# Kernel optimization log

Hardware: AMD Instinct MI355X
Metric: run time of the kernel (lower is better)

## Reference

```python
import jax, jax.numpy as jnp
import numpy as np

B, S, D, H, DFF, NB = 32, 512, 256, 8, 1024, 2
L = NB + 2 * NB  # 2 blocks_1 + 4 blocks_2 = 6 layers, params stacked on axis 0
DK = D // H
NEG = jnp.float32(-1e32)


def _ln(x, s, b):
    mu = jnp.mean(x, -1, keepdims=True)
    var = jnp.mean((x - mu) ** 2, -1, keepdims=True)
    return (x - mu) * jax.lax.rsqrt(var + 1e-5) * s + b


def _attn(q, k, v, gamma, mask, zero_pad):
    # q,k,v: [B,H,S,DK]; mask: [1,1,S,S] bool; gamma: [H,1,1]
    scores = jnp.einsum('bhid,bhjd->bhij', q, k) / jnp.float32(np.sqrt(DK))
    # distance-decay effect (computed with no grad in the original)
    sc = jax.nn.softmax(jnp.where(mask, scores, NEG), axis=-1) * mask
    cum = jnp.cumsum(sc, axis=-1)
    tot = jnp.sum(sc, axis=-1, keepdims=True)
    idx = jnp.arange(S, dtype=jnp.float32)
    pos = jnp.abs(idx[None, :] - idx[:, None])[None, None]  # |i-j|
    dist = jax.lax.stop_gradient(jnp.sqrt(jnp.maximum((tot - cum) * pos, 0.0)))
    g = -jax.nn.softplus(gamma)[None]  # [1,H,1,1]
    eff = jnp.clip(jnp.exp(dist * g), 1e-5, 1e5)
    scores = jnp.where(mask, scores * eff, NEG)
    a = jax.nn.softmax(scores, axis=-1)
    if zero_pad:
        a = a.at[:, :, 0, :].set(0.0)
    return jnp.einsum('bhij,bhjd->bhid', a, v)


def _layer(i, mask_flag, q, k, v, apply_pos,
           Wk, bk, Wv, bv, Wo, bo, gammas, ln1_s, ln1_b, W1, b1, W2, b2, ln2_s, ln2_b):
    diag = 0 if mask_flag == 1 else -1  # mask=1: incl. diag; mask=0: strictly past
    mask = jnp.tril(jnp.ones((S, S), bool), diag)[None, None]
    to_h = lambda x, W, bb: (x @ W + bb).reshape(B, S, H, DK).transpose(0, 2, 1, 3)
    qh = to_h(q, Wk[i], bk[i])  # kq_same=True -> q uses k_linear
    kh = to_h(k, Wk[i], bk[i])
    vh = to_h(v, Wv[i], bv[i])
    o = _attn(qh, kh, vh, gammas[i], mask, zero_pad=(mask_flag == 0))
    o = o.transpose(0, 2, 1, 3).reshape(B, S, D) @ Wo[i] + bo[i]
    q = _ln(q + o, ln1_s[i], ln1_b[i])
    if apply_pos:
        f = jax.nn.relu(q @ W1[i] + b1[i]) @ W2[i] + b2[i]
        q = _ln(q + f, ln2_s[i], ln2_b[i])
    return q


def _forward(q_embed_data, qa_embed_data, *p):
    y, x = qa_embed_data, q_embed_data
    for i in range(NB):
        y = _layer(i, 1, y, y, y, True, *p)
    flag = True
    for j in range(2 * NB):
        i = NB + j
        if flag:
            x = _layer(i, 1, x, x, x, False, *p)
        else:
            x = _layer(i, 0, x, x, y, True, *p)
        flag = not flag
    return x


def setup_inputs() -> dict:
    key = jax.random.key(0)
    ks = jax.random.split(key, 9)
    sd = jnp.float32(1.0 / np.sqrt(D))
    sdf = jnp.float32(1.0 / np.sqrt(DFF))
    xb = float(np.sqrt(3.0))  # xavier bound for gammas (fan_in=fan_out=1)
    return {
        'q_embed_data': jax.random.normal(ks[0], (B, S, D), jnp.float32),
        'qa_embed_data': jax.random.normal(ks[1], (B, S, D), jnp.float32),
        'Wk': jax.random.normal(ks[2], (L, D, D), jnp.float32) * sd,
        'bk': jnp.zeros((L, D), jnp.float32),
        'Wv': jax.random.normal(ks[3], (L, D, D), jnp.float32) * sd,
        'bv': jnp.zeros((L, D), jnp.float32),
        'Wo': jax.random.normal(ks[4], (L, D, D), jnp.float32) * sd,
        'bo': jnp.zeros((L, D), jnp.float32),
        'gammas': jax.random.uniform(ks[5], (L, H, 1, 1), jnp.float32, -xb, xb),
        'ln1_s': jnp.ones((L, D), jnp.float32),
        'ln1_b': jnp.zeros((L, D), jnp.float32),
        'W1': jax.random.normal(ks[6], (L, D, DFF), jnp.float32) * sd,
        'b1': jnp.zeros((L, DFF), jnp.float32),
        'W2': jax.random.normal(ks[7], (L, DFF, D), jnp.float32) * sdf,
        'b2': jnp.zeros((L, D), jnp.float32),
        'ln2_s': jnp.ones((L, D), jnp.float32),
        'ln2_b': jnp.zeros((L, D), jnp.float32),
    }


def reference(q_embed_data, qa_embed_data, Wk, bk, Wv, bv, Wo, bo, gammas,
              ln1_s, ln1_b, W1, b1, W2, b2, ln2_s, ln2_b):
    return _forward(q_embed_data, qa_embed_data, Wk, bk, Wv, bv, Wo, bo, gammas,
                    ln1_s, ln1_b, W1, b1, W2, b2, ln2_s, ln2_b)
```

## Files before the change

kernel.cpp:

```cpp
#include <hip/hip_runtime.h>
#include <cstdint>
#include <cstddef>


#define AS1 __attribute__((address_space(1)))
#define AS3 __attribute__((address_space(3)))

typedef __bf16 bf16;
typedef __bf16 bf16x8 __attribute__((ext_vector_type(8)));
typedef __bf16 bf16x4 __attribute__((ext_vector_type(4)));
typedef __bf16 bf16x2 __attribute__((ext_vector_type(2)));
typedef float  f32x4  __attribute__((ext_vector_type(4)));
typedef float  f32x16 __attribute__((ext_vector_type(16)));
typedef unsigned int u32;

static constexpr int Mc = 32 * 512;

__global__ void cvt_copy2_kernel(const float* __restrict__ s0, float* __restrict__ da32,
                                 bf16* __restrict__ da16, const float* __restrict__ s1,
                                 float* __restrict__ db32, bf16* __restrict__ db16, int n4) {
  const float* s = blockIdx.y ? s1 : s0;
  float* d32 = blockIdx.y ? db32 : da32;
  bf16* d16 = blockIdx.y ? db16 : da16;
  int i = blockIdx.x * blockDim.x + threadIdx.x;
  if (i < n4) {
    float4 v = ((const float4*)s)[i];
    ((float4*)d32)[i] = v;
    bf16x4 hx = {(bf16)v.x, (bf16)v.y, (bf16)v.z, (bf16)v.w};
    ((bf16x4*)d16)[i] = hx;
  }
}

__global__ __launch_bounds__(256) void transpose_cvt_all(
    const float* __restrict__ Wk, const float* __restrict__ Wv, const float* __restrict__ Wo,
    const float* __restrict__ W1, const float* __restrict__ W2,
    bf16* __restrict__ Wkt, bf16* __restrict__ Wvt, bf16* __restrict__ Wot,
    bf16* __restrict__ W1t, bf16* __restrict__ W2t) {
  int z = blockIdx.z;
  int layer = z % 6, w = z / 6;
  const float* src; bf16* dst; int K, N;
  switch (w) {
    case 0: src = Wk; dst = Wkt; K = 256; N = 256; break;
    case 1: src = Wv; dst = Wvt; K = 256; N = 256; break;
    case 2: src = Wo; dst = Wot; K = 256; N = 256; break;
    case 3: src = W1; dst = W1t; K = 256; N = 1024; break;
    default: src = W2; dst = W2t; K = 1024; N = 256; break;
  }
  int k0 = blockIdx.x * 64, n0 = blockIdx.y * 64;
  if (k0 >= K || n0 >= N) return;
  src += (size_t)layer * K * N;
  dst += (size_t)layer * K * N;
  __shared__ bf16 t[64][68];
  int tid = threadIdx.x;
  int rr = tid >> 4;
  int c4 = (tid & 15) * 4;
#pragma unroll
  for (int p = 0; p < 4; ++p) {
    int k = rr + p * 16;
    float4 v = *(const float4*)(src + (size_t)(k0 + k) * N + n0 + c4);
    t[c4 + 0][k] = (bf16)v.x;
    t[c4 + 1][k] = (bf16)v.y;
    t[c4 + 2][k] = (bf16)v.z;
    t[c4 + 3][k] = (bf16)v.w;
  }
  __syncthreads();
#pragma unroll
  for (int p = 0; p < 4; ++p) {
    int nl = rr + p * 16;
    bf16x4 o4 = *(const bf16x4*)&t[nl][c4];
    *(bf16x4*)(dst + (size_t)(n0 + nl) * K + k0 + c4) = o4;
  }
}

template <int RELU, typename OUT_T>
__device__ __forceinline__ void gemm_body(
    const bf16* __restrict__ A, const bf16* __restrict__ Bt,
    const float* __restrict__ bias, OUT_T* __restrict__ C,
    int K, int N, int m0, int n0, bf16* As, bf16* Bs) {
  const int tid = threadIdx.x;
  const int lane = tid & 63;
  const int wid = tid >> 6;
  const int wm = (wid >> 1) * 64;
  const int wn = (wid & 1) * 64;
  f32x4 acc[4][4] = {};

  const int o1 = wid * 1024 + lane * 16;
  const int o2 = o1 + 4096;
  const int r1 = o1 >> 6, c1 = o1 & 63;
  const int r2 = o2 >> 6, c2 = o2 & 63;
  const char* Ab = (const char*)A;
  const char* Bb = (const char*)Bt;
  const size_t stride = (size_t)K * 2;

  auto stage = [&](int buf, int kk) {
    const char* a1 = Ab + (size_t)(m0 + r1) * stride + (size_t)kk * 2 + c1;
    const char* a2 = Ab + (size_t)(m0 + r2) * stride + (size_t)kk * 2 + c2;
    const char* b1 = Bb + (size_t)(n0 + r1) * stride + (size_t)kk * 2 + c1;
    const char* b2 = Bb + (size_t)(n0 + r2) * stride + (size_t)kk * 2 + c2;
    char* ad = (char*)As + buf * 8192 + wid * 1024;
    char* bd = (char*)Bs + buf * 8192 + wid * 1024;
    __builtin_amdgcn_global_load_lds((const AS1 u32*)a1, (AS3 u32*)ad, 16, 0, 0);
    __builtin_amdgcn_global_load_lds((const AS1 u32*)a2, (AS3 u32*)(ad + 4096), 16, 0, 0);
    __builtin_amdgcn_global_load_lds((const AS1 u32*)b1, (AS3 u32*)bd, 16, 0, 0);
    __builtin_amdgcn_global_load_lds((const AS1 u32*)b2, (AS3 u32*)(bd + 4096), 16, 0, 0);
  };

  stage(0, 0);
  asm volatile("s_waitcnt vmcnt(0)" ::: "memory");
  __syncthreads();

  int cur = 0;
  for (int k0 = 0; k0 < K; k0 += 32) {
    if (k0 + 32 < K) stage(cur ^ 1, k0 + 32);
    const int rr = lane & 15;
    const int g8 = (lane >> 4) * 8;
    const int base = cur * 4096;
    bf16x8 af[4], bfr[4];
#pragma unroll
    for (int i = 0; i < 4; ++i) {
      af[i]  = *(const bf16x8*)&As[base + (wm + i * 16 + rr) * 32 + g8];
      bfr[i] = *(const bf16x8*)&Bs[base + (wn + i * 16 + rr) * 32 + g8];
    }
#pragma unroll
    for (int mi = 0; mi < 4; ++mi)
#pragma unroll
      for (int ni = 0; ni < 4; ++ni)
        acc[mi][ni] = __builtin_amdgcn_mfma_f32_16x16x32_bf16(af[mi], bfr[ni], acc[mi][ni], 0, 0, 0);
    asm volatile("s_waitcnt vmcnt(0)" ::: "memory");
    __syncthreads();
    cur ^= 1;
  }

  const int rr = lane & 15;
  const int g4 = (lane >> 4) * 4;
  float bv[4];
#pragma unroll
  for (int ni = 0; ni < 4; ++ni) bv[ni] = bias[n0 + wn + ni * 16 + rr];
#pragma unroll
  for (int mi = 0; mi < 4; ++mi)
#pragma unroll
    for (int ni = 0; ni < 4; ++ni)
#pragma unroll
      for (int r = 0; r < 4; ++r) {
        float v = acc[mi][ni][r] + bv[ni];
        if (RELU) v = fmaxf(v, 0.f);
        int row = m0 + wm + mi * 16 + g4 + r;
        int col = n0 + wn + ni * 16 + rr;
        C[(size_t)row * N + col] = (OUT_T)v;
      }
}

template <int RELU, typename OUT_T>
__global__ __launch_bounds__(256) void gemm_bias_kernel(
    const bf16* __restrict__ A, const bf16* __restrict__ Bt,
    const float* __restrict__ bias, OUT_T* __restrict__ C, int K, int N) {
  __shared__ bf16 As[2 * 128 * 32];
  __shared__ bf16 Bs[2 * 128 * 32];
  gemm_body<RELU, OUT_T>(A, Bt, bias, C, K, N, blockIdx.x * 128, blockIdx.y * 128, As, Bs);
}

__global__ __launch_bounds__(256) void gemm_kv_kernel(
    const bf16* __restrict__ A0, const bf16* __restrict__ Bt0,
    const float* __restrict__ b0, bf16* __restrict__ C0,
    const bf16* __restrict__ A1, const bf16* __restrict__ Bt1,
    const float* __restrict__ b1, bf16* __restrict__ C1, int K, int N) {
  __shared__ bf16 As[2 * 128 * 32];
  __shared__ bf16 Bs[2 * 128 * 32];
  int sel = blockIdx.y >> 1;
  gemm_body<0, bf16>(sel ? A1 : A0, sel ? Bt1 : Bt0, sel ? b1 : b0, sel ? C1 : C0,
                     K, N, blockIdx.x * 128, (blockIdx.y & 1) * 128, As, Bs);
}

template <int KSZ>
__global__ __launch_bounds__(512, 4) void gemm_ln_kernel(
    const bf16* __restrict__ A, const bf16* __restrict__ Bt,
    const float* __restrict__ bias, const float* __restrict__ resid,
    const float* __restrict__ lns, const float* __restrict__ lnb,
    float* __restrict__ out32, bf16* __restrict__ out16) {
  __shared__ bf16 As[2 * 32 * 32];
  __shared__ bf16 Bs[2 * 256 * 32];
  __shared__ float wsum[8][16][2];
  __shared__ float stats[32][2];
  const int tid = threadIdx.x, lane = tid & 63, wid = tid >> 6;
  const int m0 = blockIdx.x * 32;
  const int wr = wid >> 2, wc = wid & 3;
  f32x4 acc[4] = {};
  const char* Ab = (const char*)A;
  const char* Bb = (const char*)Bt;
  const size_t stride = (size_t)KSZ * 2;

  auto stage = [&](int buf, int kk) {
    if (wid < 2) {
      int off = wid * 1024 + lane * 16;
      const char* a1 = Ab + (size_t)(m0 + (off >> 6)) * stride + (size_t)kk * 2 + (off & 63);
      __builtin_amdgcn_global_load_lds((const AS1 u32*)a1,
                                       (AS3 u32*)((char*)As + buf * 2048 + wid * 1024), 16, 0, 0);
    }
    int off1 = wid * 2048 + lane * 16;
    int off2 = off1 + 1024;
    const char* b1 = Bb + (size_t)(off1 >> 6) * stride + (size_t)kk * 2 + (off1 & 63);
    const char* b2 = Bb + (size_t)(off2 >> 6) * stride + (size_t)kk * 2 + (off2 & 63);
    char* bd = (char*)Bs + buf * 16384 + wid * 2048;
    __builtin_amdgcn_global_load_lds((const AS1 u32*)b1, (AS3 u32*)bd, 16, 0, 0);
    __builtin_amdgcn_global_load_lds((const AS1 u32*)b2, (AS3 u32*)(bd + 1024), 16, 0, 0);
  };

  stage(0, 0);
  asm volatile("s_waitcnt vmcnt(0)" ::: "memory");
  __syncthreads();

  int cur = 0;
  for (int k0 = 0; k0 < KSZ; k0 += 32) {
    if (k0 + 32 < KSZ) stage(cur ^ 1, k0 + 32);
    const int rr = lane & 15, g8 = (lane >> 4) * 8;
    bf16x8 af = *(const bf16x8*)&As[cur * 1024 + (wr * 16 + rr) * 32 + g8];
    bf16x8 bfr[4];
#pragma unroll
    for (int ni = 0; ni < 4; ++ni)
      bfr[ni] = *(const bf16x8*)&Bs[cur * 8192 + (wc * 64 + ni * 16 + rr) * 32 + g8];
#pragma unroll
    for (int ni = 0; ni < 4; ++ni)
      acc[ni] = __builtin_amdgcn_mfma_f32_16x16x32_bf16(af, bfr[ni], acc[ni], 0, 0, 0);
    asm volatile("s_waitcnt vmcnt(0)" ::: "memory");
    __syncthreads();
    cur ^= 1;
  }

  const int rr = lane & 15, g4 = (lane >> 4) * 4;
  float bv[4], scv[4], biv[4];
  int col[4];
#pragma unroll
  for (int ni = 0; ni < 4; ++ni) {
    col[ni] = wc * 64 + ni * 16 + rr;
    bv[ni] = bias[col[ni]];
    scv[ni] = lns[col[ni]];
    biv[ni] = lnb[col[ni]];
  }
  float v[4][4];
#pragma unroll
  for (int r = 0; r < 4; ++r) {
    int grow = m0 + wr * 16 + g4 + r;
#pragma unroll
    for (int ni = 0; ni < 4; ++ni)
      v[ni][r] = acc[ni][r] + bv[ni] + resid[(size_t)grow * 256 + col[ni]];
  }
#pragma unroll
  for (int r = 0; r < 4; ++r) {
    float s1 = (v[0][r] + v[1][r]) + (v[2][r] + v[3][r]);
    float s2 = (v[0][r] * v[0][r] + v[1][r] * v[1][r]) + (v[2][r] * v[2][r] + v[3][r] * v[3][r]);
#pragma unroll
    for (int off = 8; off; off >>= 1) {
      s1 += __shfl_xor(s1, off);
      s2 += __shfl_xor(s2, off);
    }
    if (rr == 0) {
      int lrow = wr * 16 + g4 + r;
      wsum[wid][lrow & 15][0] = s1;
      wsum[wid][lrow & 15][1] = s2;
    }
  }
  __syncthreads();
  if (tid < 32) {
    int row = tid;
    int band = row >> 4;
    float s1 = 0.f, s2 = 0.f;
#pragma unroll
    for (int k = 0; k < 4; ++k) {
      s1 += wsum[band * 4 + k][row & 15][0];
      s2 += wsum[band * 4 + k][row & 15][1];
    }
    float mu = s1 * (1.f / 256.f);
    float var = s2 * (1.f / 256.f) - mu * mu;
    stats[row][0] = mu;
    stats[row][1] = rsqrtf(var + 1e-5f);
  }
  __syncthreads();
#pragma unroll
  for (int r = 0; r < 4; ++r) {
    int lrow = wr * 16 + g4 + r;
    int grow = m0 + lrow;
    float mu = stats[lrow][0], rs = stats[lrow][1];
#pragma unroll
    for (int ni = 0; ni < 4; ++ni) {
      float y = (v[ni][r] - mu) * rs * scv[ni] + biv[ni];
      out32[(size_t)grow * 256 + col[ni]] = y;
      out16[(size_t)grow * 256 + col[ni]] = (bf16)y;
    }
  }
}

static constexpr int LDK = 34;
static constexpr int LDV = 534;
static constexpr float LOG2E = 1.4426950408889634f;
static constexpr float KSC = 0.17677669529663687f * LOG2E;

__device__ __forceinline__ int jloc(int r, int hi) { return (r & 3) + 8 * (r >> 2) + 4 * hi; }

__device__ __forceinline__ u32 pkbf(float x, float y) {
  bf16x2 t = {(bf16)x, (bf16)y};
  return __builtin_bit_cast(u32, t);
}

__device__ __forceinline__ void plswap(u32& a, u32& b) {
  asm volatile("v_permlane32_swap_b32 %0, %1" : "+v"(a), "+v"(b));
}

__device__ __forceinline__ f32x16 qk_tile(const bf16* Klds, int jbase, int lq,
                                          const bf16x8& qf0, const bf16x8& qf1, int hi) {
  const bf16x8 ka0 = *(const bf16x8*)&Klds[(jbase + lq) * LDK + hi * 8];
  const bf16x8 ka1 = *(const bf16x8*)&Klds[(jbase + lq) * LDK + 16 + hi * 8];
  f32x16 c = {};
  c = __builtin_amdgcn_mfma_f32_32x32x16_bf16(ka0, qf0, c, 0, 0, 0);
  c = __builtin_amdgcn_mfma_f32_32x32x16_bf16(ka1, qf1, c, 0, 0, 0);
  return c;
}

template <bool MASKED>
__device__ __forceinline__ void tileA(const f32x16& c, int jbase, int hi, int qlim, float& tot) {
  float t[4] = {0.f, 0.f, 0.f, 0.f};
#pragma unroll
  for (int q2 = 0; q2 < 4; ++q2)
#pragma unroll
    for (int p = 0; p < 4; ++p) {
      const int r = q2 * 4 + p;
      float e = __builtin_amdgcn_exp2f(c[r] * KSC);
      if (MASKED) {
        int j = jbase + 8 * q2 + 4 * hi + p;
        if (j > qlim) e = 0.f;
      }
      t[q2] += e;
    }
  tot += (t[0] + t[1]) + (t[2] + t[3]);
}

template <bool MASKED>
__device__ __forceinline__ void tileB(const f32x16& c, int jbase, int lq, int hi,
                                      int qlim, float itot, float gneg2, float posf,
                                      const bf16* Vt, float& run, float& sum2, f32x16& pvacc) {
  float su2[16], lcs[16], G[4];
#pragma unroll
  for (int q2 = 0; q2 < 4; ++q2) {
    float a = 0.f;
#pragma unroll
    for (int p = 0; p < 4; ++p) {
      const int r = q2 * 4 + p;
      su2[r] = c[r] * KSC;
      float e = __builtin_amdgcn_exp2f(su2[r]);
      if (MASKED) {
        int j = jbase + 8 * q2 + 4 * hi + p;
        if (j > qlim) e = 0.f;
      }
      a += e;
      lcs[r] = a;
    }
    G[q2] = a;
  }
  float Po[4];
#pragma unroll
  for (int q2 = 0; q2 < 4; ++q2) Po[q2] = __shfl_xor(G[q2], 32);
  float base[4];
  {
    float pre = run;
#pragma unroll
    for (int q2 = 0; q2 < 4; ++q2) {
      base[q2] = pre + (hi ? Po[q2] : 0.f);
      pre += G[q2] + Po[q2];
    }
    run = pre;
  }
#pragma unroll
  for (int cc = 0; cc < 2; ++cc) {
    float pv[8];
#pragma unroll
    for (int q2s = 0; q2s < 2; ++q2s) {
      const int q2 = cc * 2 + q2s;
#pragma unroll
      for (int p = 0; p < 4; ++p) {
        const int r = q2 * 4 + p;
        float cum = base[q2] + lcs[r];
        float pos = posf - (float)(8 * q2 + p);
        float d2 = fmaxf(__builtin_fmaf(-cum, itot, 1.f) * pos, 0.f);
        float dist = __builtin_amdgcn_sqrtf(d2);
        float eff = fmaxf(__builtin_amdgcn_exp2f(dist * gneg2), 1e-5f);
        float t = __builtin_amdgcn_exp2f(su2[r] * eff);
        if (MASKED) {
          int j = jbase + 8 * q2 + 4 * hi + p;
          if (j > qlim) t = 0.f;
        }
        pv[q2s * 4 + p] = t;
      }
    }
    sum2 += ((pv[0] + pv[1]) + (pv[2] + pv[3])) + ((pv[4] + pv[5]) + (pv[6] + pv[7]));
    u32 a0 = pkbf(pv[0], pv[1]);
    u32 a1 = pkbf(pv[2], pv[3]);
    u32 b0 = pkbf(pv[4], pv[5]);
    u32 b1 = pkbf(pv[6], pv[7]);
    plswap(a0, b0);
    plswap(a1, b1);
    uint4 fq; fq.x = a0; fq.y = a1; fq.z = b0; fq.w = b1;
    bf16x8 pa = __builtin_bit_cast(bf16x8, fq);
    bf16x8 vb = *(const bf16x8*)&Vt[(size_t)lq * LDV + jbase + cc * 16 + hi * 8];
    pvacc = __builtin_amdgcn_mfma_f32_32x32x16_bf16(pa, vb, pvacc, 0, 0, 0);
  }
}

__global__ __launch_bounds__(1024, 4) void attn_kernel(
    const bf16* __restrict__ kh, const bf16* __restrict__ vh,
    const float* __restrict__ gam, bf16* __restrict__ o, int incl_diag) {
  __shared__ bf16 Klds[512 * LDK];
  __shared__ bf16 Vt[32 * LDV];

  const int tid = threadIdx.x;
  const int lane = tid & 63;
  const int wid = tid >> 6;
  const int bh = blockIdx.x;
  const int b = bh >> 3, h = bh & 7;
  const bf16* kbase = kh + ((size_t)b * 4096 + h) * 32;
  const bf16* vbase = vh + ((size_t)b * 4096 + h) * 32;
  bf16* obase = o + ((size_t)b * 4096 + h) * 32;

#pragma unroll
  for (int it = 0; it < 2; ++it) {
    int t = it * 1024 + tid;
    int j = t >> 2, cc = t & 3;
    bf16x8 kv8 = *(const bf16x8*)(kbase + (size_t)j * 256 + cc * 8);
    *(bf16x8*)&Klds[j * LDK + cc * 8] = kv8;
  }
  {
    int u = tid & 255;
    int cg = tid >> 8;
    const bf16* vb = vbase + (size_t)(2 * u) * 256 + cg * 8;
    bf16x8 r0 = *(const bf16x8*)(vb);
    bf16x8 r1 = *(const bf16x8*)(vb + 256);
#pragma unroll
    for (int e = 0; e < 8; ++e) {
      bf16x2 w2 = {r0[e], r1[e]};
      *(bf16x2*)&Vt[(size_t)(cg * 8 + e) * LDV + 2 * u] = w2;
    }
  }
  __syncthreads();

  float gm = gam[h];
  float gneg = -(fmaxf(gm, 0.f) + log1pf(__expf(-fabsf(gm))));
  const float gneg2 = gneg * LOG2E;
  const int lq = lane & 31;
  const int hi = lane >> 5;

  const int k = wid & 3, gsel = wid >> 2;
  int qb;
  switch (gsel) {
    case 0: qb = k; break;
    case 1: qb = 7 - k; break;
    case 2: qb = 8 + k; break;
    default: qb = 15 - k; break;
  }
  const int q0 = qb * 32;
  const int qr = q0 + lq;
  const int qlim = incl_diag ? qr : qr - 1;

  const bf16x8 qf0 = *(const bf16x8*)&Klds[(q0 + lq) * LDK + hi * 8];
  const bf16x8 qf1 = *(const bf16x8*)&Klds[(q0 + lq) * LDK + 16 + hi * 8];

  float tot = 0.f;
  {
    f32x16 c = qk_tile(Klds, 0, lq, qf0, qf1, hi);
    for (int jt = 0; jt < qb; ++jt) {
      f32x16 cn = qk_tile(Klds, (jt + 1) * 32, lq, qf0, qf1, hi);
      tileA<false>(c, jt * 32, hi, qlim, tot);
      c = cn;
    }
    tileA<true>(c, q0, hi, qlim, tot);
  }
  tot += __shfl_xor(tot, 32);
  const float itot = tot > 0.f ? 1.f / tot : 0.f;

  float run = 0.f, sum2 = 0.f;
  f32x16 pvacc = {};
  float posf = (float)(qr - 4 * hi);
  {
    f32x16 c = qk_tile(Klds, 0, lq, qf0, qf1, hi);
    for (int jt = 0; jt < qb; ++jt) {
      f32x16 cn = qk_tile(Klds, (jt + 1) * 32, lq, qf0, qf1, hi);
      tileB<false>(c, jt * 32, lq, hi, qlim, itot, gneg2, posf, Vt, run, sum2, pvacc);
      posf -= 32.f;
      c = cn;
    }
    tileB<true>(c, q0, lq, hi, qlim, itot, gneg2, posf, Vt, run, sum2, pvacc);
  }
  sum2 += __shfl_xor(sum2, 32);
  const float inv2 = sum2 > 0.f ? 1.f / sum2 : 0.f;

#pragma unroll
  for (int r = 0; r < 16; ++r) {
    int qv = jloc(r, hi);
    float iv = __shfl(inv2, qv);
    obase[(size_t)(q0 + qv) * 256 + lq] = (bf16)(pvacc[r] * iv);
  }
}

extern "C" void kernel_launch(void* const* d_in, const int* in_sizes, int n_in,
                              void* d_out, int out_size, void* d_ws, size_t ws_size,
                              hipStream_t stream) {
  const float* q_embed  = (const float*)d_in[0];
  const float* qa_embed = (const float*)d_in[1];
  const float* Wk = (const float*)d_in[2];
  const float* bk = (const float*)d_in[3];
  const float* Wv = (const float*)d_in[4];
  const float* bv = (const float*)d_in[5];
  const float* Wo = (const float*)d_in[6];
  const float* bo = (const float*)d_in[7];
  const float* gammas = (const float*)d_in[8];
  const float* ln1_s = (const float*)d_in[9];
  const float* ln1_b = (const float*)d_in[10];
  const float* W1 = (const float*)d_in[11];
  const float* b1 = (const float*)d_in[12];
  const float* W2 = (const float*)d_in[13];
  const float* b2 = (const float*)d_in[14];
  const float* ln2_s = (const float*)d_in[15];
  const float* ln2_b = (const float*)d_in[16];
  float* out = (float*)d_out;

  char* ws = (char*)d_ws;
  float* y32 = (float*)(ws);
  float* x32 = (float*)(ws + ((size_t)16 << 20));
  bf16* y16  = (bf16*)(ws + ((size_t)32 << 20));
  bf16* x16  = (bf16*)(ws + ((size_t)40 << 20));
  bf16* khb  = (bf16*)(ws + ((size_t)48 << 20));
  bf16* vhb  = (bf16*)(ws + ((size_t)56 << 20));
  bf16* o16  = (bf16*)(ws + ((size_t)64 << 20));
  bf16* h116 = (bf16*)(ws + ((size_t)88 << 20));
  bf16* Wkt  = (bf16*)(ws + ((size_t)122 << 20));
  bf16* Wvt  = Wkt + 6 * 65536;
  bf16* Wot  = Wvt + 6 * 65536;
  bf16* W1t  = Wot + 6 * 65536;
  bf16* W2t  = W1t + 6 * 262144;

  transpose_cvt_all<<<dim3(16, 16, 30), 256, 0, stream>>>(Wk, Wv, Wo, W1, W2,
                                                          Wkt, Wvt, Wot, W1t, W2t);
  cvt_copy2_kernel<<<dim3(4096, 2), 256, 0, stream>>>(q_embed, x32, x16,
                                                      qa_embed, y32, y16, Mc * 256 / 4);

  for (int i = 0; i < 6; ++i) {
    const bool first = (i < 2);
    const bool strict = (i == 3 || i == 5);
    const bool pos = first || strict;
    bf16* in16 = first ? y16 : x16;
    bf16* v16  = (first || strict) ? y16 : x16;
    float* res32 = first ? y32 : x32;

    gemm_kv_kernel<<<dim3(128, 4), 256, 0, stream>>>(
        in16, Wkt + (size_t)i * 65536, bk + i * 256, khb,
        v16, Wvt + (size_t)i * 65536, bv + i * 256, vhb, 256, 256);
    attn_kernel<<<256, 1024, 0, stream>>>(khb, vhb, gammas + i * 8, o16, strict ? 0 : 1);
    gemm_ln_kernel<256><<<512, 512, 0, stream>>>(
        o16, Wot + (size_t)i * 65536, bo + i * 256, res32,
        ln1_s + i * 256, ln1_b + i * 256, res32, in16);
    if (pos) {
      gemm_bias_kernel<1, bf16><<<dim3(128, 8), 256, 0, stream>>>(
          in16, W1t + (size_t)i * 262144, b1 + i * 1024, h116, 256, 1024);
      float* fin = (i == 5) ? out : res32;
      gemm_ln_kernel<1024><<<512, 512, 0, stream>>>(
          h116, W2t + (size_t)i * 262144, b2 + i * 256, res32,
          ln2_s + i * 256, ln2_b + i * 256, fin, in16);
    }
  }
}
```

Before: 614.7 us.

## Split high query tiles across wave pairs to balance causal attention work

Replaces the static wave-to-query-block assignment with a pairing scheme. Each front wave handles a low query block and also the first part of the key range for a high query block. The paired back wave handles the rest of that high block's key range. Partial row sums, normaliser sums and PV accumulators are exchanged through shared memory with two block barriers. This evens out per-wave work under the causal mask, at the cost of extra LDS (a 32x32 float tile per pair), extra barriers, and dropping the software prefetch of the next QK tile.

Measured after the change: 600.6 us. 2.3% less time.

```diff
diff --git a/kernel.cpp b/kernel.cpp
--- a/kernel.cpp
+++ b/kernel.cpp
@@ -409,6 +409,10 @@
     const float* __restrict__ gam, bf16* __restrict__ o, int incl_diag) {
   __shared__ bf16 Klds[512 * LDK];
   __shared__ bf16 Vt[32 * LDV];
+  __shared__ float exA[8][32];
+  __shared__ float exB[8][32];
+  __shared__ float s2A[8][32];
+  __shared__ float pvp[8][32][32];
 
   const int tid = threadIdx.x;
   const int lane = tid & 63;
@@ -446,55 +450,120 @@
   const int lq = lane & 31;
   const int hi = lane >> 5;
 
-  const int k = wid & 3, gsel = wid >> 2;
-  int qb;
-  switch (gsel) {
-    case 0: qb = k; break;
-    case 1: qb = 7 - k; break;
-    case 2: qb = 8 + k; break;
-    default: qb = 15 - k; break;
-  }
-  const int q0 = qb * 32;
-  const int qr = q0 + lq;
-  const int qlim = incl_diag ? qr : qr - 1;
-
-  const bf16x8 qf0 = *(const bf16x8*)&Klds[(q0 + lq) * LDK + hi * 8];
-  const bf16x8 qf1 = *(const bf16x8*)&Klds[(q0 + lq) * LDK + 16 + hi * 8];
-
-  float tot = 0.f;
-  {
-    f32x16 c = qk_tile(Klds, 0, lq, qf0, qf1, hi);
-    for (int jt = 0; jt < qb; ++jt) {
-      f32x16 cn = qk_tile(Klds, (jt + 1) * 32, lq, qf0, qf1, hi);
-      tileA<false>(c, jt * 32, hi, qlim, tot);
-      c = cn;
-    }
-    tileA<true>(c, q0, hi, qlim, tot);
-  }
-  tot += __shfl_xor(tot, 32);
-  const float itot = tot > 0.f ? 1.f / tot : 0.f;
-
-  float run = 0.f, sum2 = 0.f;
-  f32x16 pvacc = {};
-  float posf = (float)(qr - 4 * hi);
-  {
-    f32x16 c = qk_tile(Klds, 0, lq, qf0, qf1, hi);
-    for (int jt = 0; jt < qb; ++jt) {
-      f32x16 cn = qk_tile(Klds, (jt + 1) * 32, lq, qf0, qf1, hi);
-      tileB<false>(c, jt * 32, lq, hi, qlim, itot, gneg2, posf, Vt, run, sum2, pvacc);
+  const int p = wid & 7;
+  const bool front = wid < 8;
+  const int f = 7 - p;
+  const int qbHi = 15 - p;
+  const int ntHi = 16 - p;
+  const int q0Hi = qbHi * 32;
+  const int qrHi = q0Hi + lq;
+  const int qlimHi = incl_diag ? qrHi : qrHi - 1;
+  const int q0Lo = p * 32;
+  const int qrLo = q0Lo + lq;
+  const int qlimLo = incl_diag ? qrLo : qrLo - 1;
+
+  const bf16x8 qfH0 = *(const bf16x8*)&Klds[(q0Hi + lq) * LDK + hi * 8];
+  const bf16x8 qfH1 = *(const bf16x8*)&Klds[(q0Hi + lq) * LDK + 16 + hi * 8];
+
+  float totLo = 0.f, S = 0.f;
+  if (front) {
+    const bf16x8 qfL0 = *(const bf16x8*)&Klds[(q0Lo + lq) * LDK + hi * 8];
+    const bf16x8 qfL1 = *(const bf16x8*)&Klds[(q0Lo + lq) * LDK + 16 + hi * 8];
+    for (int jt = 0; jt < p; ++jt) {
+      f32x16 c = qk_tile(Klds, jt * 32, lq, qfL0, qfL1, hi);
+      tileA<false>(c, jt * 32, hi, qlimLo, totLo);
+    }
+    {
+      f32x16 c = qk_tile(Klds, q0Lo, lq, qfL0, qfL1, hi);
+      tileA<true>(c, q0Lo, hi, qlimLo, totLo);
+    }
+    totLo += __shfl_xor(totLo, 32);
+    for (int jt = 0; jt < f; ++jt) {
+      f32x16 c = qk_tile(Klds, jt * 32, lq, qfH0, qfH1, hi);
+      tileA<false>(c, jt * 32, hi, qlimHi, S);
+    }
+    S += __shfl_xor(S, 32);
+    if (lane < 32) exA[p][lq] = S;
+  } else {
+    for (int jt = f; jt < ntHi - 1; ++jt) {
+      f32x16 c = qk_tile(Klds, jt * 32, lq, qfH0, qfH1, hi);
+      tileA<false>(c, jt * 32, hi, qlimHi, S);
+    }
+    {
+      f32x16 c = qk_tile(Klds, q0Hi, lq, qfH0, qfH1, hi);
+      tileA<true>(c, q0Hi, hi, qlimHi, S);
+    }
+    S += __shfl_xor(S, 32);
+    if (lane < 32) exB[p][lq] = S;
+  }
+  __syncthreads();
+  const float SA = exA[p][lq];
+  const float SB = exB[p][lq];
+  const float totHi = SA + SB;
+  const float itotHi = totHi > 0.f ? 1.f / totHi : 0.f;
+
+  f32x16 pvHi = {};
+  float sum2Hi = 0.f;
+  if (front) {
+    const bf16x8 qfL0 = *(const bf16x8*)&Klds[(q0Lo + lq) * LDK + hi * 8];
+    const bf16x8 qfL1 = *(const bf16x8*)&Klds[(q0Lo + lq) * LDK + 16 + hi * 8];
+    const float itotLo = totLo > 0.f ? 1.f / totLo : 0.f;
+    f32x16 pvLo = {};
+    float sum2Lo = 0.f, run = 0.f;
+    float posf = (float)(qrLo - 4 * hi);
+    for (int jt = 0; jt < p; ++jt) {
+      f32x16 c = qk_tile(Klds, jt * 32, lq, qfL0, qfL1, hi);
+      tileB<false>(c, jt * 32, lq, hi, qlimLo, itotLo, gneg2, posf, Vt, run, sum2Lo, pvLo);
       posf -= 32.f;
-      c = cn;
-    }
-    tileB<true>(c, q0, lq, hi, qlim, itot, gneg2, posf, Vt, run, sum2, pvacc);
-  }
-  sum2 += __shfl_xor(sum2, 32);
-  const float inv2 = sum2 > 0.f ? 1.f / sum2 : 0.f;
-
-#pragma unroll
-  for (int r = 0; r < 16; ++r) {
-    int qv = jloc(r, hi);
-    float iv = __shfl(inv2, qv);
-    obase[(size_t)(q0 + qv) * 256 + lq] = (bf16)(pvacc[r] * iv);
+    }
+    {
+      f32x16 c = qk_tile(Klds, q0Lo, lq, qfL0, qfL1, hi);
+      tileB<true>(c, q0Lo, lq, hi, qlimLo, itotLo, gneg2, posf, Vt, run, sum2Lo, pvLo);
+    }
+    sum2Lo += __shfl_xor(sum2Lo, 32);
+    const float inv2Lo = sum2Lo > 0.f ? 1.f / sum2Lo : 0.f;
+#pragma unroll
+    for (int r = 0; r < 16; ++r) {
+      int qv = jloc(r, hi);
+      float iv = __shfl(inv2Lo, qv);
+      obase[(size_t)(q0Lo + qv) * 256 + lq] = (bf16)(pvLo[r] * iv);
+    }
+    run = 0.f;
+    posf = (float)(qrHi - 4 * hi);
+    for (int jt = 0; jt < f; ++jt) {
+      f32x16 c = qk_tile(Klds, jt * 32, lq, qfH0, qfH1, hi);
+      tileB<false>(c, jt * 32, lq, hi, qlimHi, itotHi, gneg2, posf, Vt, run, sum2Hi, pvHi);
+      posf -= 32.f;
+    }
+    sum2Hi += __shfl_xor(sum2Hi, 32);
+    if (lane < 32) s2A[p][lq] = sum2Hi;
+#pragma unroll
+    for (int r = 0; r < 16; ++r) pvp[p][jloc(r, hi)][lq] = pvHi[r];
+  } else {
+    float run = SA;
+    float posf = (float)(qrHi - 4 * hi - 32 * f);
+    for (int jt = f; jt < ntHi - 1; ++jt) {
+      f32x16 c = qk_tile(Klds, jt * 32, lq, qfH0, qfH1, hi);
+      tileB<false>(c, jt * 32, lq, hi, qlimHi, itotHi, gneg2, posf, Vt, run, sum2Hi, pvHi);
+      posf -= 32.f;
+    }
+    {
+      f32x16 c = qk_tile(Klds, q0Hi, lq, qfH0, qfH1, hi);
+      tileB<true>(c, q0Hi, lq, hi, qlimHi, itotHi, gneg2, posf, Vt, run, sum2Hi, pvHi);
+    }
+    sum2Hi += __shfl_xor(sum2Hi, 32);
+  }
+  __syncthreads();
+  if (!front) {
+    const float s2 = s2A[p][lq] + sum2Hi;
+    const float inv2 = s2 > 0.f ? 1.f / s2 : 0.f;
+#pragma unroll
+    for (int r = 0; r < 16; ++r) {
+      int qv = jloc(r, hi);
+      float iv = __shfl(inv2, qv);
+      float val = pvHi[r] + pvp[p][qv][lq];
+      obase[(size_t)(q0Hi + qv) * 256 + lq] = (bf16)(val * iv);
+    }
   }
 }
 
```
